# Kernel optimization log

Measured on AMD Instinct MI355X. Metric: run time of the kernel, lower is better.

The kernel has to match this reference:

```python
import jax, jax.numpy as jnp
import numpy as np
from jax import lax

B, T = 128, 512
V, D = 100000, 100   # word vocab, word embedding dim
H = 100              # per-direction LSTM hidden (concat -> 200)
L = 25               # number of CRF labels


def setup_inputs() -> dict:
    key = jax.random.key(0)
    ks = jax.random.split(key, 16)
    s = 0.02
    inp = {
        "tok_tensor": jax.random.randint(ks[0], (B, T), 0, V, dtype=jnp.int32),
        "tag_tensor": jax.random.randint(ks[1], (B, T), 0, L, dtype=jnp.int32),
        "lengths": jnp.full((B,), T, dtype=jnp.int32),
        "word_emb": jax.random.normal(ks[2], (V, D), jnp.float32) * s,
        # forward-direction LSTM (PyTorch gate order i,f,g,o)
        "w_ih_f": jax.random.normal(ks[3], (4 * H, D), jnp.float32) * s,
        "w_hh_f": jax.random.normal(ks[4], (4 * H, H), jnp.float32) * s,
        "b_ih_f": jax.random.normal(ks[5], (4 * H,), jnp.float32) * s,
        "b_hh_f": jax.random.normal(ks[6], (4 * H,), jnp.float32) * s,
        # backward-direction LSTM
        "w_ih_b": jax.random.normal(ks[7], (4 * H, D), jnp.float32) * s,
        "w_hh_b": jax.random.normal(ks[8], (4 * H, H), jnp.float32) * s,
        "b_ih_b": jax.random.normal(ks[9], (4 * H,), jnp.float32) * s,
        "b_hh_b": jax.random.normal(ks[10], (4 * H,), jnp.float32) * s,
        # hidden2tag linear
        "w_tag": jax.random.normal(ks[11], (L, 2 * H), jnp.float32) * s,
        "b_tag": jax.random.normal(ks[12], (L,), jnp.float32) * s,
        # CRF params
        "transitions": jax.random.normal(ks[13], (L, L), jnp.float32) * 0.1,
        "start_trans": jax.random.normal(ks[14], (L,), jnp.float32) * 0.1,
        "end_trans": jax.random.normal(ks[15], (L,), jnp.float32) * 0.1,
    }
    return inp


def _lstm(x_tbd, w_ih, w_hh, b_ih, b_hh, reverse):
    """x_tbd: [T,B,D] -> hidden states [T,B,H], aligned with input time axis."""
    Bh = x_tbd.shape[1]
    Hh = w_hh.shape[1]
    h0 = jnp.zeros((Bh, Hh), x_tbd.dtype)
    c0 = jnp.zeros((Bh, Hh), x_tbd.dtype)

    def step(carry, xt):
        h, c = carry
        gates = xt @ w_ih.T + b_ih + h @ w_hh.T + b_hh
        i, f, g, o = jnp.split(gates, 4, axis=-1)
        i = jax.nn.sigmoid(i); f = jax.nn.sigmoid(f)
        g = jnp.tanh(g); o = jax.nn.sigmoid(o)
        c = f * c + i * g
        h = o * jnp.tanh(c)
        return (h, c), h

    _, hs = lax.scan(step, (h0, c0), x_tbd, reverse=reverse)
    return hs


def _crf_nll(emissions, tags, mask, transitions, start_trans, end_trans):
    """Sum over batch of -(gold path score - log partition).
    emissions: [B,T,L], tags: [B,T] int, mask: [B,T] float (1=valid)."""
    Bb = emissions.shape[0]
    b_idx = jnp.arange(Bb)
    em_t = emissions.transpose(1, 0, 2)   # [T,B,L]
    tags_t = tags.T                       # [T,B]
    mask_t = mask.T                       # [T,B]

    # --- gold path score ---
    first_tags = tags_t[0]
    score0 = start_trans[first_tags] + em_t[0][b_idx, first_tags]

    def num_step(score, inp):
        em, tp, tc, m = inp  # emissions[t], tags[t-1], tags[t], mask[t]
        s = transitions[tp, tc] + em[b_idx, tc]
        return score + m * s, None

    gold, _ = lax.scan(num_step, score0,
                       (em_t[1:], tags_t[:-1], tags_t[1:], mask_t[1:]))
    last_idx = jnp.sum(mask, axis=1).astype(jnp.int32) - 1
    last_tags = tags[b_idx, last_idx]
    gold = gold + end_trans[last_tags]

    # --- log partition (forward algorithm) ---
    alpha0 = start_trans + em_t[0]  # [B,L]

    def part_step(alpha, inp):
        em, m = inp
        # [B,L_prev,1] + [L_prev,L_next] + [B,1,L_next]
        nxt = jax.nn.logsumexp(alpha[:, :, None] + transitions[None] + em[:, None, :], axis=1)
        alpha = jnp.where(m[:, None] > 0, nxt, alpha)
        return alpha, None

    alpha, _ = lax.scan(part_step, alpha0, (em_t[1:], mask_t[1:]))
    logZ = jax.nn.logsumexp(alpha + end_trans, axis=1)
    return jnp.sum(logZ - gold)


def reference(tok_tensor, tag_tensor, lengths,
              word_emb, w_ih_f, w_hh_f, b_ih_f, b_hh_f,
              w_ih_b, w_hh_b, b_ih_b, b_hh_b,
              w_tag, b_tag, transitions, start_trans, end_trans):
    # word embedding lookup: [B,T,D]
    tok_embs = word_emb[tok_tensor]
    x_tbd = tok_embs.transpose(1, 0, 2)  # [T,B,D]
    # BiLSTM encoder (dropout off: eval / deterministic reference)
    h_fwd = _lstm(x_tbd, w_ih_f, w_hh_f, b_ih_f, b_hh_f, reverse=False)
    h_bwd = _lstm(x_tbd, w_ih_b, w_hh_b, b_ih_b, b_hh_b, reverse=True)
    seq = jnp.concatenate([h_fwd, h_bwd], axis=-1).transpose(1, 0, 2)  # [B,T,2H]
    # hidden2tag
    emissions = jnp.einsum('btd,ld->btl', seq, w_tag) + b_tag  # [B,T,L]
    # CRF negative log-likelihood
    mask = (jnp.arange(T)[None, :] < lengths[:, None]).astype(emissions.dtype)
    return _crf_nll(emissions, tag_tensor, mask, transitions, start_trans, end_trans)
```

## Files before the change

### kernel.cpp

```cpp
#include <hip/hip_runtime.h>
#include <cstdint>
#include <cstddef>

#define BB 128
#define TT 512
#define DD 100
#define HH 100
#define NG 400
#define LL 25
#define TS 32
#define NTILE 16
#define F_LOG2E 1.44269504088896340736f
#define F_LN2   0.69314718055994530942f

typedef __decltype(__builtin_amdgcn_cvt_pkrtz(0.f, 0.f)) h2_t;
typedef _Float16 v8h __attribute__((ext_vector_type(8)));
typedef float v4f __attribute__((ext_vector_type(4)));

__device__ __forceinline__ h2_t bc_h2(unsigned int u) {
  return __builtin_bit_cast(h2_t, u);
}
__device__ __forceinline__ unsigned int pk(float x, float y) {
  return __builtin_bit_cast(unsigned int, __builtin_amdgcn_cvt_pkrtz(x, y));
}
__device__ __forceinline__ unsigned int pk_rte(float x, float y) {
  unsigned short a = __builtin_bit_cast(unsigned short, (__fp16)x);
  unsigned short c = __builtin_bit_cast(unsigned short, (__fp16)y);
  return (unsigned int)a | ((unsigned int)c << 16);
}

__device__ __forceinline__ float fdot2(h2_t a, h2_t b, float c) {
#if __has_builtin(__builtin_amdgcn_fdot2)
  return __builtin_amdgcn_fdot2(a, b, c, false);
#else
  return c + (float)a[0] * (float)b[0] + (float)a[1] * (float)b[1];
#endif
}

__device__ __forceinline__ float fexp2(float x) { return __builtin_amdgcn_exp2f(x); }
__device__ __forceinline__ float flog2(float x) { return __builtin_amdgcn_logf(x); }
__device__ __forceinline__ float frcp(float x)  { return __builtin_amdgcn_rcpf(x); }

__device__ __forceinline__ float sigmoid_f(float x) {
  return frcp(1.f + fexp2(-F_LOG2E * x));
}
__device__ __forceinline__ float tanh_f(float x) {
  float e = fexp2(2.f * F_LOG2E * x);
  return 1.f - 2.f * frcp(e + 1.f);
}

template <int CTRL>
__device__ __forceinline__ float qadd(float v) {
#if __has_builtin(__builtin_amdgcn_mov_dpp)
  int m = __builtin_amdgcn_mov_dpp(__builtin_bit_cast(int, v), CTRL, 0xF, 0xF, true);
  return v + __builtin_bit_cast(float, m);
#else
  int x = (CTRL == 177) ? 1 : 2;
  return v + __shfl_xor(v, x);
#endif
}

template <int LANE>
__device__ __forceinline__ float qbcast(float v) {
#if __has_builtin(__builtin_amdgcn_mov_dpp)
  int m = __builtin_amdgcn_mov_dpp(__builtin_bit_cast(int, v), LANE * 0x55, 0xF, 0xF, true);
  return __builtin_bit_cast(float, m);
#else
  return __shfl(v, (threadIdx.x & 63 & ~3) + LANE);
#endif
}

__device__ __forceinline__ float rfl(float v) {
  return __builtin_bit_cast(float,
      __builtin_amdgcn_readfirstlane(__builtin_bit_cast(int, v)));
}

__device__ __forceinline__ void wave_fence() {
#if __has_builtin(__builtin_amdgcn_wave_barrier)
  __builtin_amdgcn_wave_barrier();
#endif
}

__device__ __forceinline__ void lds_barrier() {
  __builtin_amdgcn_s_waitcnt(0xC07F);
  __builtin_amdgcn_s_barrier();
}

__global__ __launch_bounds__(512, 2) void lstm_fused4(
    const int* __restrict__ tok, const float* __restrict__ emb,
    const float* __restrict__ w_ih_f, const float* __restrict__ w_ih_b,
    const float* __restrict__ b_ih_f, const float* __restrict__ b_hh_f,
    const float* __restrict__ b_ih_b, const float* __restrict__ b_hh_b,
    const float* __restrict__ w_hh_f, const float* __restrict__ w_hh_b,
    const float* __restrict__ w_tag, const float* __restrict__ b_tag,
    float* __restrict__ em_f, float* __restrict__ em_b)
{
  const int tid = threadIdx.x;
  const int b   = blockIdx.x & 127;
  const int dir = blockIdx.x >> 7;
  const float* w_hh = dir ? w_hh_b : w_hh_f;
  const float* w_ih = dir ? w_ih_b : w_ih_f;
  const float* b_ih = dir ? b_ih_b : b_ih_f;
  const float* b_hh = dir ? b_hh_b : b_hh_f;
  float* emo = dir ? em_b : em_f;

  __shared__ __align__(16) unsigned short gin_lds[TS * 400];
  __shared__ __align__(16) unsigned int xlds[TS * 68];
  __shared__ __align__(16) unsigned int hhist[TS * 68];
  __shared__ __align__(16) unsigned int hls0[56];
  __shared__ __align__(16) unsigned int hls1[56];

  const int wv   = tid >> 6;
  const int lane = tid & 63;
  const int l16  = lane & 15;
  const int quad = lane >> 4;
  const int c0b  = (25 * wv) >> 3;
  const int c1b  = (25 * (wv + 1)) >> 3;
  const int ncol = c1b - c0b;

  v8h bfr[4][4];
  int pcol[4];
#pragma unroll
  for (int ci = 0; ci < 4; ++ci) {
    const int cc = (ci < ncol) ? (c0b + ci) : c0b;
    const int n  = 16 * cc + l16;
    const float* wr = w_ih + (size_t)n * DD;
#pragma unroll
    for (int f = 0; f < 3; ++f) {
      const float* wp = wr + f * 32 + quad * 8;
      float4 va = *(const float4*)(wp);
      float4 vb = *(const float4*)(wp + 4);
      uint4 u;
      u.x = pk(va.x, va.y); u.y = pk(va.z, va.w);
      u.z = pk(vb.x, vb.y); u.w = pk(vb.z, vb.w);
      bfr[ci][f] = __builtin_bit_cast(v8h, u);
    }
    {
      uint4 u = {0u, 0u, 0u, 0u};
      if (quad == 0) {
        float4 va = *(const float4*)(wr + 96);
        u.x = pk(va.x, va.y); u.y = pk(va.z, va.w);
      }
      bfr[ci][3] = __builtin_bit_cast(v8h, u);
    }
    const int qn = (n * 41) >> 12;
    pcol[ci] = ((n - 100 * qn) << 2) + qn;
  }

  for (int i = tid; i < TS * 18; i += 512) {
    int row = i / 18;
    int d = i - row * 18;
    xlds[row * 68 + 50 + d] = 0u;
    hhist[row * 68 + 50 + d] = 0u;
  }

  const bool uact = tid < 200;
  const int j  = tid >> 1;
  const int s2 = tid & 1;

  h2_t wG0[25], wG1[25], wG2[25], wG3[25];
  float bias0 = 0.f, bias1 = 0.f, bias2 = 0.f, bias3 = 0.f;
  if (uact) {
    const float* r0 = w_hh + (size_t)(0 * 100 + j) * HH + 50 * s2;
    const float* r1 = w_hh + (size_t)(1 * 100 + j) * HH + 50 * s2;
    const float* r2 = w_hh + (size_t)(2 * 100 + j) * HH + 50 * s2;
    const float* r3 = w_hh + (size_t)(3 * 100 + j) * HH + 50 * s2;
#pragma unroll
    for (int d = 0; d < 25; ++d) {
      float2 v0 = *(const float2*)(r0 + 2 * d);
      float2 v1 = *(const float2*)(r1 + 2 * d);
      float2 v2 = *(const float2*)(r2 + 2 * d);
      float2 v3 = *(const float2*)(r3 + 2 * d);
      wG0[d] = __builtin_amdgcn_cvt_pkrtz(v0.x, v0.y);
      wG1[d] = __builtin_amdgcn_cvt_pkrtz(v1.x, v1.y);
      wG2[d] = __builtin_amdgcn_cvt_pkrtz(v2.x, v2.y);
      wG3[d] = __builtin_amdgcn_cvt_pkrtz(v3.x, v3.y);
    }
    bias0 = b_ih[j]       + b_hh[j];
    bias1 = b_ih[100 + j] + b_hh[100 + j];
    bias2 = b_ih[200 + j] + b_hh[200 + j];
    bias3 = b_ih[300 + j] + b_hh[300 + j];
  }

  const int ew    = wv - 4;
  const int ecb   = ew & 1;
  const int erg   = (ew >> 1) & 1;
  const int encol = 16 * ecb + l16;
  const bool eact2 = (wv >= 4) && (encol < LL);
  v8h etag[4];
  float ebias = 0.f;
  if (wv >= 4) {
#pragma unroll
    for (int f = 0; f < 3; ++f) {
      uint4 u = {0u, 0u, 0u, 0u};
      if (eact2) {
        const float* wp = w_tag + (size_t)encol * 200 + dir * 100 + f * 32 + quad * 8;
        float4 va = *(const float4*)(wp);
        float4 vb = *(const float4*)(wp + 4);
        u.x = pk(va.x, va.y); u.y = pk(va.z, va.w);
        u.z = pk(vb.x, vb.y); u.w = pk(vb.z, vb.w);
      }
      etag[f] = __builtin_bit_cast(v8h, u);
    }
    {
      uint4 u = {0u, 0u, 0u, 0u};
      if (eact2 && quad == 0) {
        float4 va = *(const float4*)(w_tag + (size_t)encol * 200 + dir * 100 + 96);
        u.x = pk(va.x, va.y); u.y = pk(va.z, va.w);
      }
      etag[3] = __builtin_bit_cast(v8h, u);
    }
    if (eact2 && dir == 0) ebias = b_tag[encol];
  }

  if (tid < 56) { hls0[tid] = 0u; hls1[tid] = 0u; }

  const int tprow = tid / 13;
  const int tps   = tid - 13 * tprow;
  const bool tp_act = tid < 416;

  float4 xa = {0, 0, 0, 0}, xb = {0, 0, 0, 0};
  if (tp_act) {
    int ii = tprow;
    int tt = dir ? (TT - 1 - ii) : ii;
    int tk = tok[b * TT + tt];
    const float* xp = emb + (size_t)tk * DD + 8 * tps;
    xa = *(const float4*)xp;
    if (tps < 12) xb = *(const float4*)(xp + 4);
  }

  float c = 0.f;
  uint2 gnext = {0u, 0u};

#define SD2(d, hw) { h2_t hv = bc_h2(hw);                                  \
  p0 = fdot2(wG0[d], hv, p0); p1 = fdot2(wG1[d], hv, p1);                  \
  p2 = fdot2(wG2[d], hv, p2); p3 = fdot2(wG3[d], hv, p3); }

#define SCAN2(HRD, HWR, ROW)                                               \
  {                                                                        \
    if (uact) {                                                            \
      uint2 gcurr = gnext;                                                 \
      int nr = ((ROW) < TS - 1) ? (ROW) + 1 : TS - 1;                      \
      gnext = ((const uint2*)(gin_lds + nr * 400))[j];                     \
      const unsigned int* hp = (HRD) + 28 * s2;                            \
      uint4 u0 = *((const uint4*)hp);                                      \
      uint4 u1 = *((const uint4*)(hp + 4));                                \
      uint4 u2 = *((const uint4*)(hp + 8));                                \
      uint4 u3 = *((const uint4*)(hp + 12));                               \
      uint4 u4 = *((const uint4*)(hp + 16));                               \
      uint4 u5 = *((const uint4*)(hp + 20));                               \
      unsigned int u6 = hp[24];                                            \
      float p0 = 0.f, p1 = 0.f, p2 = 0.f, p3 = 0.f;                        \
      SD2(0, u0.x)  SD2(1, u0.y)  SD2(2, u0.z)  SD2(3, u0.w)               \
      SD2(4, u1.x)  SD2(5, u1.y)  SD2(6, u1.z)  SD2(7, u1.w)               \
      SD2(8, u2.x)  SD2(9, u2.y)  SD2(10, u2.z) SD2(11, u2.w)              \
      SD2(12, u3.x) SD2(13, u3.y) SD2(14, u3.z) SD2(15, u3.w)              \
      SD2(16, u4.x) SD2(17, u4.y) SD2(18, u4.z) SD2(19, u4.w)              \
      SD2(20, u5.x) SD2(21, u5.y) SD2(22, u5.z) SD2(23, u5.w)              \
      SD2(24, u6)                                                          \
      p0 = qadd<177>(p0); p1 = qadd<177>(p1);                              \
      p2 = qadd<177>(p2); p3 = qadd<177>(p3);                              \
      h2_t glo = bc_h2(gcurr.x), ghi = bc_h2(gcurr.y);                     \
      float gi = p0 + bias0 + (float)glo[0];                               \
      float gf = p1 + bias1 + (float)glo[1];                               \
      float gg = p2 + bias2 + (float)ghi[0];                               \
      float go = p3 + bias3 + (float)ghi[1];                               \
      float iv = sigmoid_f(gi);                                            \
      float fv = sigmoid_f(gf);                                            \
      float gv = tanh_f(gg);                                               \
      float ov = sigmoid_f(go);                                            \
      c = fmaf(fv, c, iv * gv);                                            \
      float hvv = ov * tanh_f(c);                                          \
      float hnb = qbcast<2>(hvv);                                          \
      if ((tid & 3) == 0) {                                                \
        int k = tid >> 2;                                                  \
        unsigned int val = pk_rte(hvv, hnb);                               \
        (HWR)[k + (k >= 25 ? 3 : 0)] = val;                                \
        hhist[(ROW) * 68 + k] = val;                                       \
      }                                                                    \
    }                                                                      \
    lds_barrier();                                                         \
  }

#define EMIT_GEMM(TB)                                                      \
  {                                                                        \
    const unsigned int* hb = hhist + (erg * 16 + l16) * 68 + quad * 4;     \
    v8h ah0 = __builtin_bit_cast(v8h, *(const uint4*)(hb));                \
    v8h ah1 = __builtin_bit_cast(v8h, *(const uint4*)(hb + 16));           \
    v8h ah2 = __builtin_bit_cast(v8h, *(const uint4*)(hb + 32));           \
    v8h ah3 = __builtin_bit_cast(v8h, *(const uint4*)(hb + 48));           \
    v4f ea = {0.f, 0.f, 0.f, 0.f};                                         \
    ea = __builtin_amdgcn_mfma_f32_16x16x32_f16(ah0, etag[0], ea, 0, 0, 0);\
    ea = __builtin_amdgcn_mfma_f32_16x16x32_f16(ah1, etag[1], ea, 0, 0, 0);\
    ea = __builtin_amdgcn_mfma_f32_16x16x32_f16(ah2, etag[2], ea, 0, 0, 0);\
    ea = __builtin_amdgcn_mfma_f32_16x16x32_f16(ah3, etag[3], ea, 0, 0, 0);\
    if (eact2) {                                                           \
      const int tb = (TB) + erg * 16 + quad * 4;                           \
      _Pragma("unroll")                                                    \
      for (int r = 0; r < 4; ++r) {                                        \
        int t = dir ? (TT - 1 - (tb + r)) : (tb + r);                      \
        emo[((size_t)b * TT + t) * LL + encol] = ea[r] + ebias;            \
      }                                                                    \
    }                                                                      \
  }

  __syncthreads();

  for (int T = 0; T < NTILE; ++T) {
    if (tp_act) {
      unsigned int* xr = xlds + tprow * 68 + 4 * tps;
      if (tps < 12) {
        uint4 u;
        u.x = pk(xa.x, xa.y); u.y = pk(xa.z, xa.w);
        u.z = pk(xb.x, xb.y); u.w = pk(xb.z, xb.w);
        *(uint4*)xr = u;
      } else {
        xr[0] = pk(xa.x, xa.y);
        xr[1] = pk(xa.z, xa.w);
      }
    }
    __syncthreads();

    {
      v8h af[2][4];
#pragma unroll
      for (int rg = 0; rg < 2; ++rg)
#pragma unroll
        for (int f = 0; f < 4; ++f)
          af[rg][f] = __builtin_bit_cast(v8h,
              *(const uint4*)(xlds + (rg * 16 + l16) * 68 + f * 16 + quad * 4));

      if (tp_act && T + 1 < NTILE) {
        int ii = (T + 1) * TS + tprow;
        int tt = dir ? (TT - 1 - ii) : ii;
        int tk = tok[b * TT + tt];
        const float* xp = emb + (size_t)tk * DD + 8 * tps;
        xa = *(const float4*)xp;
        if (tps < 12) xb = *(const float4*)(xp + 4);
      }

      __fp16* gout = (__fp16*)gin_lds;
#pragma unroll
      for (int ci = 0; ci < 4; ++ci) {
        if (ci >= ncol) break;
        const int p = pcol[ci];
#pragma unroll
        for (int rg = 0; rg < 2; ++rg) {
          v4f acc = {0.f, 0.f, 0.f, 0.f};
          acc = __builtin_amdgcn_mfma_f32_16x16x32_f16(af[rg][0], bfr[ci][0], acc, 0, 0, 0);
          acc = __builtin_amdgcn_mfma_f32_16x16x32_f16(af[rg][1], bfr[ci][1], acc, 0, 0, 0);
          acc = __builtin_amdgcn_mfma_f32_16x16x32_f16(af[rg][2], bfr[ci][2], acc, 0, 0, 0);
          acc = __builtin_amdgcn_mfma_f32_16x16x32_f16(af[rg][3], bfr[ci][3], acc, 0, 0, 0);
          const int rowb = rg * 16 + quad * 4;
#pragma unroll
          for (int r = 0; r < 4; ++r)
            gout[(rowb + r) * 400 + p] = (__fp16)acc[r];
        }
      }

      if (wv >= 4 && T > 0) {
        EMIT_GEMM((T - 1) * TS)
      }
    }
    __syncthreads();
    if (uact) gnext = ((const uint2*)gin_lds)[j];

    for (int it = 0; it < TS; it += 2) {
      SCAN2(hls0, hls1, it)
      SCAN2(hls1, hls0, it + 1)
    }
  }

  if (wv >= 4) {
    EMIT_GEMM((NTILE - 1) * TS)
  }
#undef EMIT_GEMM
#undef SCAN2
#undef SD2
}

#define CHN  8
#define CLEN 64
__device__ __align__(16) float g_PT[(size_t)BB * CHN * LL * 28];

__global__ __launch_bounds__(128, 2) void crf_chunks(
    const float* __restrict__ em_f, const float* __restrict__ em_b,
    const float* __restrict__ trans)
{
  const int tid = threadIdx.x;
  const int b   = blockIdx.x >> 3;
  const int c   = blockIdx.x & 7;
  const int ts  = c * CLEN;

  __shared__ __align__(16) float Al[2][LL][28];
  __shared__ __align__(16) float el[CLEN][32];

  {
    const int row  = tid >> 1;
    const int half = tid & 1;
    const int jb   = half ? 13 : 0;
    const int nj   = half ? 12 : 13;
    const float* pf = em_f + ((size_t)b * TT + ts + row) * LL;
    const float* pb = em_b + ((size_t)b * TT + ts + row) * LL;
    for (int q = 0; q < nj; ++q) {
      int jj = jb + q;
      el[row][jj] = fexp2((pf[jj] + pb[jj]) * F_LOG2E);
    }
  }

  const bool lact = tid < 125;
  const int i  = tid / 5;
  const int jg = tid - 5 * i;
  const int j0 = 5 * jg;

  float E[25][5];
  if (lact) {
#pragma unroll
    for (int k = 0; k < 25; ++k) {
      const float* tr = trans + k * 25 + j0;
#pragma unroll
      for (int u = 0; u < 5; ++u)
        E[k][u] = fexp2(tr[u] * F_LOG2E - 5.f);
    }
#pragma unroll
    for (int u = 0; u < 5; ++u)
      Al[0][i][j0 + u] = (i == j0 + u) ? 1.f : 0.f;
  }
  __syncthreads();

  int p = 0;
  const int s0 = (c == 0) ? 1 : 0;
  for (int st = s0; st < CLEN; ++st) {
    if (lact) {
      const float* ar = &Al[p][i][0];
      float4 q0 = *(const float4*)(ar);
      float4 q1 = *(const float4*)(ar + 4);
      float4 q2 = *(const float4*)(ar + 8);
      float4 q3 = *(const float4*)(ar + 12);
      float4 q4 = *(const float4*)(ar + 16);
      float4 q5 = *(const float4*)(ar + 20);
      float a24 = ar[24];
      float e0 = el[st][j0];
      float e1 = el[st][j0 + 1];
      float e2 = el[st][j0 + 2];
      float e3 = el[st][j0 + 3];
      float e4 = el[st][j0 + 4];
      float av[25] = {q0.x, q0.y, q0.z, q0.w, q1.x, q1.y, q1.z, q1.w,
                      q2.x, q2.y, q2.z, q2.w, q3.x, q3.y, q3.z, q3.w,
                      q4.x, q4.y, q4.z, q4.w, q5.x, q5.y, q5.z, q5.w, a24};
      float c0 = 0.f, c1 = 0.f, c2 = 0.f, c3 = 0.f, c4 = 0.f;
#pragma unroll
      for (int k = 0; k < 25; ++k) {
        float avk = av[k];
        c0 = fmaf(avk, E[k][0], c0);
        c1 = fmaf(avk, E[k][1], c1);
        c2 = fmaf(avk, E[k][2], c2);
        c3 = fmaf(avk, E[k][3], c3);
        c4 = fmaf(avk, E[k][4], c4);
      }
      float* wr = &Al[p ^ 1][i][j0];
      wr[0] = c0 * e0; wr[1] = c1 * e1; wr[2] = c2 * e2;
      wr[3] = c3 * e3; wr[4] = c4 * e4;
    }
    __syncthreads();
    p ^= 1;
  }

  if (lact) {
    const size_t base = ((size_t)(b * CHN + c)) * LL;
#pragma unroll
    for (int u = 0; u < 5; ++u)
      g_PT[(base + (j0 + u)) * 28 + i] = Al[p][i][j0 + u];
  }
}

__global__ __launch_bounds__(128) void crf_combine(
    const float* __restrict__ em_f, const float* __restrict__ em_b,
    const int* __restrict__ tags, const int* __restrict__ lengths,
    const float* __restrict__ trans,
    const float* __restrict__ startt, const float* __restrict__ endt,
    float* __restrict__ out)
{
  const int tid = threadIdx.x;
  const int b   = blockIdx.x;

  __shared__ __align__(16) float Vs[28];

  if (tid < 64) {
    const int lane = tid;
    const int j = (lane < LL) ? lane : 0;
    const float* ef0 = em_f + (size_t)b * TT * LL;
    const float* eb0 = em_b + (size_t)b * TT * LL;
    float v = fexp2((startt[j] + ef0[j] + eb0[j]) * F_LOG2E);
    float C = 0.f;
    for (int c = 0; c < CHN; ++c) {
      if (lane < LL) Vs[lane] = v;
      wave_fence();
      float4 s0 = *(const float4*)(Vs);
      float4 s1 = *(const float4*)(Vs + 4);
      float4 s2 = *(const float4*)(Vs + 8);
      float4 s3 = *(const float4*)(Vs + 12);
      float4 s4 = *(const float4*)(Vs + 16);
      float4 s5 = *(const float4*)(Vs + 20);
      float s24 = Vs[24];
      wave_fence();
      const float* pr = g_PT + ((size_t)(b * CHN + c) * LL + j) * 28;
      float4 p0 = *(const float4*)(pr);
      float4 p1 = *(const float4*)(pr + 4);
      float4 p2 = *(const float4*)(pr + 8);
      float4 p3 = *(const float4*)(pr + 12);
      float4 p4 = *(const float4*)(pr + 16);
      float4 p5 = *(const float4*)(pr + 20);
      float p24 = pr[24];
      float nv = s0.x * p0.x;
      nv = fmaf(s0.y, p0.y, nv); nv = fmaf(s0.z, p0.z, nv); nv = fmaf(s0.w, p0.w, nv);
      nv = fmaf(s1.x, p1.x, nv); nv = fmaf(s1.y, p1.y, nv);
      nv = fmaf(s1.z, p1.z, nv); nv = fmaf(s1.w, p1.w, nv);
      nv = fmaf(s2.x, p2.x, nv); nv = fmaf(s2.y, p2.y, nv);
      nv = fmaf(s2.z, p2.z, nv); nv = fmaf(s2.w, p2.w, nv);
      nv = fmaf(s3.x, p3.x, nv); nv = fmaf(s3.y, p3.y, nv);
      nv = fmaf(s3.z, p3.z, nv); nv = fmaf(s3.w, p3.w, nv);
      nv = fmaf(s4.x, p4.x, nv); nv = fmaf(s4.y, p4.y, nv);
      nv = fmaf(s4.z, p4.z, nv); nv = fmaf(s4.w, p4.w, nv);
      nv = fmaf(s5.x, p5.x, nv); nv = fmaf(s5.y, p5.y, nv);
      nv = fmaf(s5.z, p5.z, nv); nv = fmaf(s5.w, p5.w, nv);
      nv = fmaf(s24, p24, nv);
      float nv0 = rfl(nv);
      int k = ((__builtin_bit_cast(int, nv0) >> 23) & 255) - 127;
      k = (k > 100) ? 100 : ((k < -100) ? -100 : k);
      float scl = __builtin_bit_cast(float, (127 - k) << 23);
      v = nv * scl;
      C += (float)k;
    }
    float term = (lane < LL) ? v * fexp2(endt[j] * F_LOG2E) : 0.f;
    for (int o = 32; o > 0; o >>= 1) term += __shfl_down(term, o);
    if (lane == 0)
      atomicAdd(out, (flog2(term) + C + 5.f * 511.f) * F_LN2);
  } else {
    const int lane = tid & 63;
    const int len = lengths[b];
    float acc = 0.f;
#pragma unroll
    for (int k = 0; k < 8; ++k) {
      int t = k * 64 + lane;
      int tg = tags[b * TT + t];
      size_t ei = ((size_t)b * TT + t) * LL + tg;
      float e = em_f[ei] + em_b[ei];
      float term;
      if (t == 0) term = startt[tg] + e;
      else        term = trans[tags[b * TT + t - 1] * LL + tg] + e;
      if (t == len - 1) term += endt[tg];
      if (t < len) acc += term;
    }
    for (int o = 32; o > 0; o >>= 1) acc += __shfl_down(acc, o);
    if (lane == 0) atomicAdd(out, -acc);
  }
}

extern "C" void kernel_launch(void* const* d_in, const int* in_sizes, int n_in,
                              void* d_out, int out_size, void* d_ws, size_t ws_size,
                              hipStream_t stream) {
  const int*   tok   = (const int*)d_in[0];
  const int*   tags  = (const int*)d_in[1];
  const int*   lens  = (const int*)d_in[2];
  const float* emb   = (const float*)d_in[3];
  const float* wif   = (const float*)d_in[4];
  const float* whf   = (const float*)d_in[5];
  const float* bif   = (const float*)d_in[6];
  const float* bhf   = (const float*)d_in[7];
  const float* wib   = (const float*)d_in[8];
  const float* whb   = (const float*)d_in[9];
  const float* bib   = (const float*)d_in[10];
  const float* bhb   = (const float*)d_in[11];
  const float* wtag  = (const float*)d_in[12];
  const float* btag  = (const float*)d_in[13];
  const float* trans = (const float*)d_in[14];
  const float* st    = (const float*)d_in[15];
  const float* en    = (const float*)d_in[16];

  char* wsb = (char*)d_ws;
  float* em_f = (float*)wsb;
  float* em_b = (float*)(wsb + 6553600);

  hipMemsetAsync(d_out, 0, sizeof(float), stream);

  lstm_fused4<<<256, 512, 0, stream>>>(tok, emb, wif, wib, bif, bhf, bib, bhb,
                                       whf, whb, wtag, btag, em_f, em_b);
  crf_chunks<<<BB * CHN, 128, 0, stream>>>(em_f, em_b, trans);
  crf_combine<<<BB, 128, 0, stream>>>(em_f, em_b, tags, lens, trans, st, en,
                                      (float*)d_out);
}
```

Before: 410.7 us.

## Split LSTM gate recurrence across 400 threads spread over all waves

The recurrent step is remapped so each hidden unit is handled by four lanes, each pair computing two of the four gates with half the weights. Active threads now span all eight waves instead of the first four, which halves per-thread dot-product work and register weight storage on the serial critical path. Gate activations are exchanged by DPP quad permutes and a single lane writes the fp16 hidden value. Launch bounds change to one block per SM, trading occupancy for more registers. The gin_lds layout is assumed to interleave gates per unit to match the new offsets, and the extra cross-lane exchange adds latency.

```diff
diff --git a/kernel.cpp b/kernel.cpp
--- a/kernel.cpp
+++ b/kernel.cpp
@@ -23,11 +23,6 @@
 __device__ __forceinline__ unsigned int pk(float x, float y) {
   return __builtin_bit_cast(unsigned int, __builtin_amdgcn_cvt_pkrtz(x, y));
 }
-__device__ __forceinline__ unsigned int pk_rte(float x, float y) {
-  unsigned short a = __builtin_bit_cast(unsigned short, (__fp16)x);
-  unsigned short c = __builtin_bit_cast(unsigned short, (__fp16)y);
-  return (unsigned int)a | ((unsigned int)c << 16);
-}
 
 __device__ __forceinline__ float fdot2(h2_t a, h2_t b, float c) {
 #if __has_builtin(__builtin_amdgcn_fdot2)
@@ -60,13 +55,14 @@
 #endif
 }
 
-template <int LANE>
-__device__ __forceinline__ float qbcast(float v) {
+template <int CTRL>
+__device__ __forceinline__ float qperm(float v) {
 #if __has_builtin(__builtin_amdgcn_mov_dpp)
-  int m = __builtin_amdgcn_mov_dpp(__builtin_bit_cast(int, v), LANE * 0x55, 0xF, 0xF, true);
+  int m = __builtin_amdgcn_mov_dpp(__builtin_bit_cast(int, v), CTRL, 0xF, 0xF, true);
   return __builtin_bit_cast(float, m);
 #else
-  return __shfl(v, (threadIdx.x & 63 & ~3) + LANE);
+  int x = (CTRL == 177) ? 1 : 2;
+  return __shfl_xor(v, x);
 #endif
 }
 
@@ -86,7 +82,7 @@
   __builtin_amdgcn_s_barrier();
 }
 
-__global__ __launch_bounds__(512, 2) void lstm_fused4(
+__global__ __launch_bounds__(512, 1) void lstm_fused6(
     const int* __restrict__ tok, const float* __restrict__ emb,
     const float* __restrict__ w_ih_f, const float* __restrict__ w_ih_b,
     const float* __restrict__ b_ih_f, const float* __restrict__ b_hh_f,
@@ -154,33 +150,33 @@
     hhist[row * 68 + 50 + d] = 0u;
   }
 
-  const bool uact = tid < 200;
-  const int j  = tid >> 1;
-  const int s2 = tid & 1;
-
-  h2_t wG0[25], wG1[25], wG2[25], wG3[25];
-  float bias0 = 0.f, bias1 = 0.f, bias2 = 0.f, bias3 = 0.f;
+  const int jl = lane >> 2;
+  const int gp = (lane >> 1) & 1;
+  const int s2 = lane & 1;
+  const int j  = 8 * jl + wv;
+  const bool uact  = (jl < 12) || (jl == 12 && wv < 4);
+  const int  goff  = 8 * j + 4 * gp;
+  const int  hidx  = j + (j >= 50 ? 6 : 0);
+
+  h2_t wA[25], wB[25];
+  float biasA = 0.f, biasB = 0.f;
   if (uact) {
-    const float* r0 = w_hh + (size_t)(0 * 100 + j) * HH + 50 * s2;
-    const float* r1 = w_hh + (size_t)(1 * 100 + j) * HH + 50 * s2;
-    const float* r2 = w_hh + (size_t)(2 * 100 + j) * HH + 50 * s2;
-    const float* r3 = w_hh + (size_t)(3 * 100 + j) * HH + 50 * s2;
+    const int g0 = 2 * gp, g1 = 2 * gp + 1;
+    const float* rA = w_hh + (size_t)(g0 * 100 + j) * HH + 50 * s2;
+    const float* rB = w_hh + (size_t)(g1 * 100 + j) * HH + 50 * s2;
 #pragma unroll
     for (int d = 0; d < 25; ++d) {
-      float2 v0 = *(const float2*)(r0 + 2 * d);
-      float2 v1 = *(const float2*)(r1 + 2 * d);
-      float2 v2 = *(const float2*)(r2 + 2 * d);
-      float2 v3 = *(const float2*)(r3 + 2 * d);
-      wG0[d] = __builtin_amdgcn_cvt_pkrtz(v0.x, v0.y);
-      wG1[d] = __builtin_amdgcn_cvt_pkrtz(v1.x, v1.y);
-      wG2[d] = __builtin_amdgcn_cvt_pkrtz(v2.x, v2.y);
-      wG3[d] = __builtin_amdgcn_cvt_pkrtz(v3.x, v3.y);
-    }
-    bias0 = b_ih[j]       + b_hh[j];
-    bias1 = b_ih[100 + j] + b_hh[100 + j];
-    bias2 = b_ih[200 + j] + b_hh[200 + j];
-    bias3 = b_ih[300 + j] + b_hh[300 + j];
-  }
+      float2 vA = *(const float2*)(rA + 2 * d);
+      float2 vB = *(const float2*)(rB + 2 * d);
+      wA[d] = __builtin_amdgcn_cvt_pkrtz(vA.x, vA.y);
+      wB[d] = __builtin_amdgcn_cvt_pkrtz(vB.x, vB.y);
+    }
+    biasA = b_ih[g0 * 100 + j] + b_hh[g0 * 100 + j];
+    biasB = b_ih[g1 * 100 + j] + b_hh[g1 * 100 + j];
+  }
+  const float kkA = gp ? (2.f * F_LOG2E) : (-F_LOG2E);
+  const float cAA = gp ? -2.f : 1.f;
+  const float cBA = gp ? 1.f : 0.f;
 
   const int ew    = wv - 4;
   const int ecb   = ew & 1;
@@ -230,18 +226,17 @@
   }
 
   float c = 0.f;
-  uint2 gnext = {0u, 0u};
+  unsigned int gnext = 0u;
 
 #define SD2(d, hw) { h2_t hv = bc_h2(hw);                                  \
-  p0 = fdot2(wG0[d], hv, p0); p1 = fdot2(wG1[d], hv, p1);                  \
-  p2 = fdot2(wG2[d], hv, p2); p3 = fdot2(wG3[d], hv, p3); }
+  pA = fdot2(wA[d], hv, pA); pB = fdot2(wB[d], hv, pB); }
 
 #define SCAN2(HRD, HWR, ROW)                                               \
   {                                                                        \
     if (uact) {                                                            \
-      uint2 gcurr = gnext;                                                 \
+      unsigned int gcurr = gnext;                                          \
       int nr = ((ROW) < TS - 1) ? (ROW) + 1 : TS - 1;                      \
-      gnext = ((const uint2*)(gin_lds + nr * 400))[j];                     \
+      gnext = *(const unsigned int*)((const char*)gin_lds + nr * 800 + goff); \
       const unsigned int* hp = (HRD) + 28 * s2;                            \
       uint4 u0 = *((const uint4*)hp);                                      \
       uint4 u1 = *((const uint4*)(hp + 4));                                \
@@ -250,7 +245,7 @@
       uint4 u4 = *((const uint4*)(hp + 16));                               \
       uint4 u5 = *((const uint4*)(hp + 20));                               \
       unsigned int u6 = hp[24];                                            \
-      float p0 = 0.f, p1 = 0.f, p2 = 0.f, p3 = 0.f;                        \
+      float pA = 0.f, pB = 0.f;                                            \
       SD2(0, u0.x)  SD2(1, u0.y)  SD2(2, u0.z)  SD2(3, u0.w)               \
       SD2(4, u1.x)  SD2(5, u1.y)  SD2(6, u1.z)  SD2(7, u1.w)               \
       SD2(8, u2.x)  SD2(9, u2.y)  SD2(10, u2.z) SD2(11, u2.w)              \
@@ -258,25 +253,25 @@
       SD2(16, u4.x) SD2(17, u4.y) SD2(18, u4.z) SD2(19, u4.w)              \
       SD2(20, u5.x) SD2(21, u5.y) SD2(22, u5.z) SD2(23, u5.w)              \
       SD2(24, u6)                                                          \
-      p0 = qadd<177>(p0); p1 = qadd<177>(p1);                              \
-      p2 = qadd<177>(p2); p3 = qadd<177>(p3);                              \
-      h2_t glo = bc_h2(gcurr.x), ghi = bc_h2(gcurr.y);                     \
-      float gi = p0 + bias0 + (float)glo[0];                               \
-      float gf = p1 + bias1 + (float)glo[1];                               \
-      float gg = p2 + bias2 + (float)ghi[0];                               \
-      float go = p3 + bias3 + (float)ghi[1];                               \
-      float iv = sigmoid_f(gi);                                            \
-      float fv = sigmoid_f(gf);                                            \
-      float gv = tanh_f(gg);                                               \
-      float ov = sigmoid_f(go);                                            \
-      c = fmaf(fv, c, iv * gv);                                            \
-      float hvv = ov * tanh_f(c);                                          \
-      float hnb = qbcast<2>(hvv);                                          \
-      if ((tid & 3) == 0) {                                                \
-        int k = tid >> 2;                                                  \
-        unsigned int val = pk_rte(hvv, hnb);                               \
-        (HWR)[k + (k >= 25 ? 3 : 0)] = val;                                \
-        hhist[(ROW) * 68 + k] = val;                                       \
+      pA = qadd<177>(pA); pB = qadd<177>(pB);                              \
+      h2_t gx = bc_h2(gcurr);                                              \
+      float gA = pA + biasA + (float)gx[0];                                \
+      float gB = pB + biasB + (float)gx[1];                                \
+      float yA = fexp2(kkA * gA);                                          \
+      float rA_ = frcp(1.f + yA);                                          \
+      float actA = fmaf(cAA, rA_, cBA);                                    \
+      float actB = sigmoid_f(gB);                                          \
+      float othA = qperm<78>(actA);                                        \
+      float othB = qperm<78>(actB);                                        \
+      float prod = actA * othA;                                            \
+      float fsel = gp ? othB : actB;                                       \
+      float osel = gp ? actB : othB;                                       \
+      c = fmaf(fsel, c, prod);                                             \
+      float hvv = osel * tanh_f(c);                                        \
+      if ((lane & 3) == 0) {                                               \
+        __fp16 hh = (__fp16)hvv;                                           \
+        ((__fp16*)(HWR))[hidx] = hh;                                       \
+        ((__fp16*)hhist)[(ROW) * 136 + j] = hh;                            \
       }                                                                    \
     }                                                                      \
     lds_barrier();                                                         \
@@ -363,7 +358,7 @@
       }
     }
     __syncthreads();
-    if (uact) gnext = ((const uint2*)gin_lds)[j];
+    if (uact) gnext = *(const unsigned int*)((const char*)gin_lds + goff);
 
     for (int it = 0; it < TS; it += 2) {
       SCAN2(hls0, hls1, it)
@@ -584,7 +579,7 @@
 
   hipMemsetAsync(d_out, 0, sizeof(float), stream);
 
-  lstm_fused4<<<256, 512, 0, stream>>>(tok, emb, wif, wib, bif, bhf, bib, bhb,
+  lstm_fused6<<<256, 512, 0, stream>>>(tok, emb, wif, wib, bif, bhf, bib, bhb,
                                        whf, whb, wtag, btag, em_f, em_b);
   crf_chunks<<<BB * CHN, 128, 0, stream>>>(em_f, em_b, trans);
   crf_combine<<<BB, 128, 0, stream>>>(em_f, em_b, tags, lens, trans, st, en,
```

Result: no change. 416.9 us (+1.5%).

## Split fused LSTM kernel into input-GEMM, lean scan, and emission kernels

Applied to the files above, without the earlier changes.

The fused per-sequence kernel, which interleaved the input projection GEMM, the recurrent scan and the emission GEMM, is replaced by three kernels. The input gates go to a global fp16 buffer, hidden states are written to global memory, and a separate kernel computes combined forward+backward emissions with MFMA. The scan kernel then runs lighter at 256 threads with no tile-level barriers or GEMM work in its serial loop. The cost is extra global traffic (about 100MB of gate values), two more launches, and a scan that reads gate inputs from global memory with only a two-step prefetch.

```diff
diff --git a/kernel.cpp b/kernel.cpp
--- a/kernel.cpp
+++ b/kernel.cpp
@@ -6,7 +6,6 @@
 #define TT 512
 #define DD 100
 #define HH 100
-#define NG 400
 #define LL 25
 #define TS 32
 #define NTILE 16
@@ -86,29 +85,23 @@
   __builtin_amdgcn_s_barrier();
 }
 
-__global__ __launch_bounds__(512, 2) void lstm_fused4(
+#define MF(a, b, c) __builtin_amdgcn_mfma_f32_16x16x32_f16(a, b, c, 0, 0, 0)
+#define LD8(base, off) __builtin_bit_cast(v8h, *(const uint4*)((base) + (off)))
+
+__device__ __align__(16) unsigned short g_gin[(size_t)2 * BB * TT * 400];
+__device__ __align__(16) unsigned int g_h2[(size_t)2 * BB * TT * 50];
+
+__global__ __launch_bounds__(512, 1) void gin_gemm(
     const int* __restrict__ tok, const float* __restrict__ emb,
-    const float* __restrict__ w_ih_f, const float* __restrict__ w_ih_b,
-    const float* __restrict__ b_ih_f, const float* __restrict__ b_hh_f,
-    const float* __restrict__ b_ih_b, const float* __restrict__ b_hh_b,
-    const float* __restrict__ w_hh_f, const float* __restrict__ w_hh_b,
-    const float* __restrict__ w_tag, const float* __restrict__ b_tag,
-    float* __restrict__ em_f, float* __restrict__ em_b)
+    const float* __restrict__ w_ih_f, const float* __restrict__ w_ih_b)
 {
   const int tid = threadIdx.x;
   const int b   = blockIdx.x & 127;
   const int dir = blockIdx.x >> 7;
-  const float* w_hh = dir ? w_hh_b : w_hh_f;
   const float* w_ih = dir ? w_ih_b : w_ih_f;
-  const float* b_ih = dir ? b_ih_b : b_ih_f;
-  const float* b_hh = dir ? b_hh_b : b_hh_f;
-  float* emo = dir ? em_b : em_f;
-
-  __shared__ __align__(16) unsigned short gin_lds[TS * 400];
+
   __shared__ __align__(16) unsigned int xlds[TS * 68];
-  __shared__ __align__(16) unsigned int hhist[TS * 68];
-  __shared__ __align__(16) unsigned int hls0[56];
-  __shared__ __align__(16) unsigned int hls1[56];
+  __shared__ __align__(16) unsigned short gt[TS * 400];
 
   const int wv   = tid >> 6;
   const int lane = tid & 63;
@@ -151,8 +144,102 @@
     int row = i / 18;
     int d = i - row * 18;
     xlds[row * 68 + 50 + d] = 0u;
-    hhist[row * 68 + 50 + d] = 0u;
-  }
+  }
+
+  const int tprow = tid / 13;
+  const int tps   = tid - 13 * tprow;
+  const bool tp_act = tid < 416;
+
+  float4 xa = {0, 0, 0, 0}, xb = {0, 0, 0, 0};
+  if (tp_act) {
+    int ii = tprow;
+    int tt = dir ? (TT - 1 - ii) : ii;
+    int tk = tok[b * TT + tt];
+    const float* xp = emb + (size_t)tk * DD + 8 * tps;
+    xa = *(const float4*)xp;
+    if (tps < 12) xb = *(const float4*)(xp + 4);
+  }
+
+  unsigned short* gout_g = g_gin + (size_t)(dir * BB + b) * TT * 400;
+  __syncthreads();
+
+  for (int T = 0; T < NTILE; ++T) {
+    if (tp_act) {
+      unsigned int* xr = xlds + tprow * 68 + 4 * tps;
+      if (tps < 12) {
+        uint4 u;
+        u.x = pk(xa.x, xa.y); u.y = pk(xa.z, xa.w);
+        u.z = pk(xb.x, xb.y); u.w = pk(xb.z, xb.w);
+        *(uint4*)xr = u;
+      } else {
+        xr[0] = pk(xa.x, xa.y);
+        xr[1] = pk(xa.z, xa.w);
+      }
+    }
+    __syncthreads();
+
+    {
+      v8h af[2][4];
+#pragma unroll
+      for (int rg = 0; rg < 2; ++rg)
+#pragma unroll
+        for (int f = 0; f < 4; ++f)
+          af[rg][f] = __builtin_bit_cast(v8h,
+              *(const uint4*)(xlds + (rg * 16 + l16) * 68 + f * 16 + quad * 4));
+
+      if (tp_act && T + 1 < NTILE) {
+        int ii = (T + 1) * TS + tprow;
+        int tt = dir ? (TT - 1 - ii) : ii;
+        int tk = tok[b * TT + tt];
+        const float* xp = emb + (size_t)tk * DD + 8 * tps;
+        xa = *(const float4*)xp;
+        if (tps < 12) xb = *(const float4*)(xp + 4);
+      }
+
+      __fp16* gout = (__fp16*)gt;
+#pragma unroll
+      for (int ci = 0; ci < 4; ++ci) {
+        if (ci >= ncol) break;
+        const int p = pcol[ci];
+#pragma unroll
+        for (int rg = 0; rg < 2; ++rg) {
+          v4f acc = {0.f, 0.f, 0.f, 0.f};
+          acc = MF(af[rg][0], bfr[ci][0], acc);
+          acc = MF(af[rg][1], bfr[ci][1], acc);
+          acc = MF(af[rg][2], bfr[ci][2], acc);
+          acc = MF(af[rg][3], bfr[ci][3], acc);
+          const int rowb = rg * 16 + quad * 4;
+#pragma unroll
+          for (int r = 0; r < 4; ++r)
+            gout[(rowb + r) * 400 + p] = (__fp16)acc[r];
+        }
+      }
+    }
+    __syncthreads();
+
+    {
+      const uint4* s = (const uint4*)gt;
+      uint4* d = (uint4*)(gout_g + (size_t)T * TS * 400);
+      for (int i = tid; i < 1600; i += 512) d[i] = s[i];
+    }
+    __syncthreads();
+  }
+}
+
+__global__ __launch_bounds__(256, 1) void scan_lean(
+    const float* __restrict__ w_hh_f, const float* __restrict__ w_hh_b,
+    const float* __restrict__ b_ih_f, const float* __restrict__ b_hh_f,
+    const float* __restrict__ b_ih_b, const float* __restrict__ b_hh_b)
+{
+  const int tid = threadIdx.x;
+  const int b   = blockIdx.x & 127;
+  const int dir = blockIdx.x >> 7;
+  const float* w_hh = dir ? w_hh_b : w_hh_f;
+  const float* b_ih = dir ? b_ih_b : b_ih_f;
+  const float* b_hh = dir ? b_hh_b : b_hh_f;
+
+  __shared__ __align__(16) unsigned int hls0[56];
+  __shared__ __align__(16) unsigned int hls1[56];
 
   const bool uact = tid < 200;
   const int j  = tid >> 1;
@@ -182,66 +269,29 @@
     bias3 = b_ih[300 + j] + b_hh[300 + j];
   }
 
-  const int ew    = wv - 4;
-  const int ecb   = ew & 1;
-  const int erg   = (ew >> 1) & 1;
-  const int encol = 16 * ecb + l16;
-  const bool eact2 = (wv >= 4) && (encol < LL);
-  v8h etag[4];
-  float ebias = 0.f;
-  if (wv >= 4) {
-#pragma unroll
-    for (int f = 0; f < 3; ++f) {
-      uint4 u = {0u, 0u, 0u, 0u};
-      if (eact2) {
-        const float* wp = w_tag + (size_t)encol * 200 + dir * 100 + f * 32 + quad * 8;
-        float4 va = *(const float4*)(wp);
-        float4 vb = *(const float4*)(wp + 4);
-        u.x = pk(va.x, va.y); u.y = pk(va.z, va.w);
-        u.z = pk(vb.x, vb.y); u.w = pk(vb.z, vb.w);
-      }
-      etag[f] = __builtin_bit_cast(v8h, u);
-    }
-    {
-      uint4 u = {0u, 0u, 0u, 0u};
-      if (eact2 && quad == 0) {
-        float4 va = *(const float4*)(w_tag + (size_t)encol * 200 + dir * 100 + 96);
-        u.x = pk(va.x, va.y); u.y = pk(va.z, va.w);
-      }
-      etag[3] = __builtin_bit_cast(v8h, u);
-    }
-    if (eact2 && dir == 0) ebias = b_tag[encol];
-  }
-
   if (tid < 56) { hls0[tid] = 0u; hls1[tid] = 0u; }
 
-  const int tprow = tid / 13;
-  const int tps   = tid - 13 * tprow;
-  const bool tp_act = tid < 416;
-
-  float4 xa = {0, 0, 0, 0}, xb = {0, 0, 0, 0};
-  if (tp_act) {
-    int ii = tprow;
-    int tt = dir ? (TT - 1 - ii) : ii;
-    int tk = tok[b * TT + tt];
-    const float* xp = emb + (size_t)tk * DD + 8 * tps;
-    xa = *(const float4*)xp;
-    if (tps < 12) xb = *(const float4*)(xp + 4);
-  }
-
+  const unsigned short* gbase = g_gin + (size_t)(dir * BB + b) * TT * 400;
+  unsigned int* ghb = g_h2 + (size_t)(dir * BB + b) * TT * 50;
+
+  uint2 ga = {0u, 0u}, gb = {0u, 0u};
+  if (uact) {
+    ga = ((const uint2*)(gbase))[j];
+    gb = ((const uint2*)(gbase + 400))[j];
+  }
   float c = 0.f;
-  uint2 gnext = {0u, 0u};
+  __syncthreads();
 
 #define SD2(d, hw) { h2_t hv = bc_h2(hw);                                  \
   p0 = fdot2(wG0[d], hv, p0); p1 = fdot2(wG1[d], hv, p1);                  \
   p2 = fdot2(wG2[d], hv, p2); p3 = fdot2(wG3[d], hv, p3); }
 
-#define SCAN2(HRD, HWR, ROW)                                               \
+#define SSTEP(T, GREG, HRD, HWR)                                           \
   {                                                                        \
     if (uact) {                                                            \
-      uint2 gcurr = gnext;                                                 \
-      int nr = ((ROW) < TS - 1) ? (ROW) + 1 : TS - 1;                      \
-      gnext = ((const uint2*)(gin_lds + nr * 400))[j];                     \
+      uint2 gcurr = GREG;                                                  \
+      int nr = ((T) + 2 < TT) ? (T) + 2 : (TT - 1);                        \
+      GREG = ((const uint2*)(gbase + (size_t)nr * 400))[j];                \
       const unsigned int* hp = (HRD) + 28 * s2;                            \
       uint4 u0 = *((const uint4*)hp);                                      \
       uint4 u1 = *((const uint4*)(hp + 4));                                \
@@ -276,107 +326,102 @@
         int k = tid >> 2;                                                  \
         unsigned int val = pk_rte(hvv, hnb);                               \
         (HWR)[k + (k >= 25 ? 3 : 0)] = val;                                \
-        hhist[(ROW) * 68 + k] = val;                                       \
+        int ta = dir ? (TT - 1 - (T)) : (T);                               \
+        ghb[(size_t)ta * 50 + k] = val;                                    \
       }                                                                    \
     }                                                                      \
     lds_barrier();                                                         \
   }
 
-#define EMIT_GEMM(TB)                                                      \
-  {                                                                        \
-    const unsigned int* hb = hhist + (erg * 16 + l16) * 68 + quad * 4;     \
-    v8h ah0 = __builtin_bit_cast(v8h, *(const uint4*)(hb));                \
-    v8h ah1 = __builtin_bit_cast(v8h, *(const uint4*)(hb + 16));           \
-    v8h ah2 = __builtin_bit_cast(v8h, *(const uint4*)(hb + 32));           \
-    v8h ah3 = __builtin_bit_cast(v8h, *(const uint4*)(hb + 48));           \
-    v4f ea = {0.f, 0.f, 0.f, 0.f};                                         \
-    ea = __builtin_amdgcn_mfma_f32_16x16x32_f16(ah0, etag[0], ea, 0, 0, 0);\
-    ea = __builtin_amdgcn_mfma_f32_16x16x32_f16(ah1, etag[1], ea, 0, 0, 0);\
-    ea = __builtin_amdgcn_mfma_f32_16x16x32_f16(ah2, etag[2], ea, 0, 0, 0);\
-    ea = __builtin_amdgcn_mfma_f32_16x16x32_f16(ah3, etag[3], ea, 0, 0, 0);\
-    if (eact2) {                                                           \
-      const int tb = (TB) + erg * 16 + quad * 4;                           \
-      _Pragma("unroll")                                                    \
-      for (int r = 0; r < 4; ++r) {                                        \
-        int t = dir ? (TT - 1 - (tb + r)) : (tb + r);                      \
-        emo[((size_t)b * TT + t) * LL + encol] = ea[r] + ebias;            \
-      }                                                                    \
-    }                                                                      \
-  }
-
+  for (int t2 = 0; t2 < TT; t2 += 2) {
+    SSTEP(t2,     ga, hls0, hls1)
+    SSTEP(t2 + 1, gb, hls1, hls0)
+  }
+#undef SSTEP
+#undef SD2
+}
+
+__global__ __launch_bounds__(256, 1) void emit_sum(
+    const float* __restrict__ w_tag, const float* __restrict__ b_tag,
+    float* __restrict__ em)
+{
+  const int tid = threadIdx.x;
+  const int b   = blockIdx.x >> 3;
+  const int tc  = blockIdx.x & 7;
+  const int t0  = tc * 64;
+
+  __shared__ __align__(16) unsigned short hb[64][256];
+
+  const int wv   = tid >> 6;
+  const int lane = tid & 63;
+  const int l16  = lane & 15;
+  const int quad = lane >> 4;
+
+  v8h wt[2][8];
+  float eb[2];
+#pragma unroll
+  for (int lt = 0; lt < 2; ++lt) {
+    const int label = lt * 16 + l16;
+    const bool valid = label < LL;
+    const float* wr = w_tag + (size_t)(valid ? label : 0) * 200;
+#pragma unroll
+    for (int kc = 0; kc < 8; ++kc) {
+      float v[8];
+#pragma unroll
+      for (int e = 0; e < 8; ++e) {
+        int k = kc * 32 + quad * 8 + e;
+        float x = 0.f;
+        if (valid) {
+          if (k < 100) x = wr[k];
+          else if (k >= 128 && k < 228) x = wr[k - 28];
+        }
+        v[e] = x;
+      }
+      uint4 u;
+      u.x = pk(v[0], v[1]); u.y = pk(v[2], v[3]);
+      u.z = pk(v[4], v[5]); u.w = pk(v[6], v[7]);
+      wt[lt][kc] = __builtin_bit_cast(v8h, u);
+    }
+    eb[lt] = valid ? b_tag[label] : 0.f;
+  }
+
+  {
+    uint4 z = {0u, 0u, 0u, 0u};
+    for (int i = tid; i < 2048; i += 256) ((uint4*)hb)[i] = z;
+  }
   __syncthreads();
-
-  for (int T = 0; T < NTILE; ++T) {
-    if (tp_act) {
-      unsigned int* xr = xlds + tprow * 68 + 4 * tps;
-      if (tps < 12) {
-        uint4 u;
-        u.x = pk(xa.x, xa.y); u.y = pk(xa.z, xa.w);
-        u.z = pk(xb.x, xb.y); u.w = pk(xb.z, xb.w);
-        *(uint4*)xr = u;
-      } else {
-        xr[0] = pk(xa.x, xa.y);
-        xr[1] = pk(xa.z, xa.w);
+  for (int i = tid; i < 64 * 2 * 13; i += 256) {
+    int row = i / 13, cp = i - 13 * row;
+    int t = row >> 1, d = row & 1;
+    const unsigned int* src = g_h2 +
+        ((size_t)(d * BB + b) * TT + t0 + t) * 50 + cp * 4;
+    char* dst = (char*)hb + t * 512 + d * 256 + cp * 16;
+    if (cp < 12) *(uint4*)dst = *(const uint4*)src;
+    else         *(uint2*)dst = *(const uint2*)src;
+  }
+  __syncthreads();
+
+  const unsigned short* hr = &hb[16 * wv + l16][0];
+  v8h ha[8];
+#pragma unroll
+  for (int kc = 0; kc < 8; ++kc)
+    ha[kc] = LD8(hr, kc * 32 + quad * 8);
+
+#pragma unroll
+  for (int lt = 0; lt < 2; ++lt) {
+    v4f acc = {0.f, 0.f, 0.f, 0.f};
+#pragma unroll
+    for (int kc = 0; kc < 8; ++kc)
+      acc = MF(ha[kc], wt[lt][kc], acc);
+    const int label = lt * 16 + l16;
+    if (label < LL) {
+#pragma unroll
+      for (int r = 0; r < 4; ++r) {
+        int t = t0 + 16 * wv + quad * 4 + r;
+        em[((size_t)b * TT + t) * LL + label] = acc[r] + eb[lt];
       }
     }
-    __syncthreads();
-
-    {
-      v8h af[2][4];
-#pragma unroll
-      for (int rg = 0; rg < 2; ++rg)
-#pragma unroll
-        for (int f = 0; f < 4; ++f)
-          af[rg][f] = __builtin_bit_cast(v8h,
-              *(const uint4*)(xlds + (rg * 16 + l16) * 68 + f * 16 + quad * 4));
-
-      if (tp_act && T + 1 < NTILE) {
-        int ii = (T + 1) * TS + tprow;
-        int tt = dir ? (TT - 1 - ii) : ii;
-        int tk = tok[b * TT + tt];
-        const float* xp = emb + (size_t)tk * DD + 8 * tps;
-        xa = *(const float4*)xp;
-        if (tps < 12) xb = *(const float4*)(xp + 4);
-      }
-
-      __fp16* gout = (__fp16*)gin_lds;
-#pragma unroll
-      for (int ci = 0; ci < 4; ++ci) {
-        if (ci >= ncol) break;
-        const int p = pcol[ci];
-#pragma unroll
-        for (int rg = 0; rg < 2; ++rg) {
-          v4f acc = {0.f, 0.f, 0.f, 0.f};
-          acc = __builtin_amdgcn_mfma_f32_16x16x32_f16(af[rg][0], bfr[ci][0], acc, 0, 0, 0);
-          acc = __builtin_amdgcn_mfma_f32_16x16x32_f16(af[rg][1], bfr[ci][1], acc, 0, 0, 0);
-          acc = __builtin_amdgcn_mfma_f32_16x16x32_f16(af[rg][2], bfr[ci][2], acc, 0, 0, 0);
-          acc = __builtin_amdgcn_mfma_f32_16x16x32_f16(af[rg][3], bfr[ci][3], acc, 0, 0, 0);
-          const int rowb = rg * 16 + quad * 4;
-#pragma unroll
-          for (int r = 0; r < 4; ++r)
-            gout[(rowb + r) * 400 + p] = (__fp16)acc[r];
-        }
-      }
-
-      if (wv >= 4 && T > 0) {
-        EMIT_GEMM((T - 1) * TS)
-      }
-    }
-    __syncthreads();
-    if (uact) gnext = ((const uint2*)gin_lds)[j];
-
-    for (int it = 0; it < TS; it += 2) {
-      SCAN2(hls0, hls1, it)
-      SCAN2(hls1, hls0, it + 1)
-    }
-  }
-
-  if (wv >= 4) {
-    EMIT_GEMM((NTILE - 1) * TS)
-  }
-#undef EMIT_GEMM
-#undef SCAN2
-#undef SD2
+  }
 }
 
 #define CHN  8
@@ -384,8 +429,7 @@
 __device__ __align__(16) float g_PT[(size_t)BB * CHN * LL * 28];
 
 __global__ __launch_bounds__(128, 2) void crf_chunks(
-    const float* __restrict__ em_f, const float* __restrict__ em_b,
-    const float* __restrict__ trans)
+    const float* __restrict__ em, const float* __restrict__ trans)
 {
   const int tid = threadIdx.x;
   const int b   = blockIdx.x >> 3;
@@ -400,11 +444,10 @@
     const int half = tid & 1;
     const int jb   = half ? 13 : 0;
     const int nj   = half ? 12 : 13;
-    const float* pf = em_f + ((size_t)b * TT + ts + row) * LL;
-    const float* pb = em_b + ((size_t)b * TT + ts + row) * LL;
+    const float* pe = em + ((size_t)b * TT + ts + row) * LL;
     for (int q = 0; q < nj; ++q) {
       int jj = jb + q;
-      el[row][jj] = fexp2((pf[jj] + pb[jj]) * F_LOG2E);
+      el[row][jj] = fexp2(pe[jj] * F_LOG2E);
     }
   }
 
@@ -475,7 +518,7 @@
 }
 
 __global__ __launch_bounds__(128) void crf_combine(
-    const float* __restrict__ em_f, const float* __restrict__ em_b,
+    const float* __restrict__ em,
     const int* __restrict__ tags, const int* __restrict__ lengths,
     const float* __restrict__ trans,
     const float* __restrict__ startt, const float* __restrict__ endt,
@@ -489,9 +532,8 @@
   if (tid < 64) {
     const int lane = tid;
     const int j = (lane < LL) ? lane : 0;
-    const float* ef0 = em_f + (size_t)b * TT * LL;
-    const float* eb0 = em_b + (size_t)b * TT * LL;
-    float v = fexp2((startt[j] + ef0[j] + eb0[j]) * F_LOG2E);
+    const float* e0p = em + (size_t)b * TT * LL;
+    float v = fexp2((startt[j] + e0p[j]) * F_LOG2E);
     float C = 0.f;
     for (int c = 0; c < CHN; ++c) {
       if (lane < LL) Vs[lane] = v;
@@ -545,7 +587,7 @@
       int t = k * 64 + lane;
       int tg = tags[b * TT + t];
       size_t ei = ((size_t)b * TT + t) * LL + tg;
-      float e = em_f[ei] + em_b[ei];
+      float e = em[ei];
       float term;
       if (t == 0) term = startt[tg] + e;
       else        term = trans[tags[b * TT + t - 1] * LL + tg] + e;
@@ -578,15 +620,14 @@
   const float* st    = (const float*)d_in[15];
   const float* en    = (const float*)d_in[16];
 
-  char* wsb = (char*)d_ws;
-  float* em_f = (float*)wsb;
-  float* em_b = (float*)(wsb + 6553600);
+  float* em = (float*)d_ws;
 
   hipMemsetAsync(d_out, 0, sizeof(float), stream);
 
-  lstm_fused4<<<256, 512, 0, stream>>>(tok, emb, wif, wib, bif, bhf, bib, bhb,
-                                       whf, whb, wtag, btag, em_f, em_b);
-  crf_chunks<<<BB * CHN, 128, 0, stream>>>(em_f, em_b, trans);
-  crf_combine<<<BB, 128, 0, stream>>>(em_f, em_b, tags, lens, trans, st, en,
+  gin_gemm<<<256, 512, 0, stream>>>(tok, emb, wif, wib);
+  scan_lean<<<256, 256, 0, stream>>>(whf, whb, bif, bhf, bib, bhb);
+  emit_sum<<<1024, 256, 0, stream>>>(wtag, btag, em);
+  crf_chunks<<<BB * CHN, 128, 0, stream>>>(em, trans);
+  crf_combine<<<BB, 128, 0, stream>>>(em, tags, lens, trans, st, en,
                                       (float*)d_out);
 }
```

Measured after the change: 492.2 us. +19.8%, slower.
